# Optimization experiments

Measured on AMD Instinct MI355X. Metric: run time of the kernel, lower is better.

## Reference

```python
import math
import jax, jax.numpy as jnp
import numpy as np

N_NODES = 50000
N_EDGES = 600000
D = 128          # in_dim == out_dim
T = 4            # num_types
R = 4            # num_relations
H = 8            # n_heads
DK = D // H
MAX_LEN = 240    # RelTemporalEncoding max_len
EPS = 1e-5


def _sinusoid_table(n_hid, max_len):
    pos = jnp.arange(max_len, dtype=jnp.float32)[:, None]
    div = jnp.exp(jnp.arange(0, n_hid, 2, dtype=jnp.float32) * (-math.log(10000.0) / n_hid))
    s = jnp.sin(pos * div) / math.sqrt(n_hid)
    c = jnp.cos(pos * div) / math.sqrt(n_hid)
    emb = jnp.zeros((max_len, n_hid), dtype=jnp.float32)
    emb = emb.at[:, 0::2].set(s).at[:, 1::2].set(c)
    return emb


def setup_inputs() -> dict:
    key = jax.random.key(0)
    ks = jax.random.split(key, 24)
    f32 = jnp.float32
    inp = {
        'node_inp': jax.random.normal(ks[0], (N_NODES, D), dtype=f32),
        'node_type': jax.random.randint(ks[1], (N_NODES,), 0, T),
        'edge_index': jax.random.randint(ks[2], (2, N_EDGES), 0, N_NODES),
        'edge_type': jax.random.randint(ks[3], (N_EDGES,), 0, R),
        'edge_time': jax.random.randint(ks[4], (N_EDGES,), 0, MAX_LEN),
        # per-type Linear weights stored as [T, in, out] (x @ W + b)
        'Wk': jax.random.normal(ks[5], (T, D, D), dtype=f32) * 0.05,
        'bk': jnp.zeros((T, D), dtype=f32),
        'Wq': jax.random.normal(ks[6], (T, D, D), dtype=f32) * 0.05,
        'bq': jnp.zeros((T, D), dtype=f32),
        'Wv': jax.random.normal(ks[7], (T, D, D), dtype=f32) * 0.05,
        'bv': jnp.zeros((T, D), dtype=f32),
        'Wa': jax.random.normal(ks[8], (T, D, D), dtype=f32) * 0.05,
        'ba': jnp.zeros((T, D), dtype=f32),
        'gamma': jnp.ones((T, D), dtype=f32),
        'beta': jnp.zeros((T, D), dtype=f32),
        'rel_pri': jnp.ones((R, H), dtype=f32),
        'rel_att': jax.random.normal(ks[9], (R, H, DK, DK), dtype=f32) * 0.1,
        'rel_msg': jax.random.normal(ks[10], (R, H, DK, DK), dtype=f32) * 0.1,
        'skip': jnp.ones((T,), dtype=f32),
        'rte_W': jax.random.normal(ks[11], (D, D), dtype=f32) * 0.05,
        'rte_b': jnp.zeros((D,), dtype=f32),
    }
    return inp


def _type_proj(x, W, b, types):
    # all-type projection [T, N, D] then gather per-node type (T is small)
    allp = jnp.einsum('ni,tio->tno', x, W) + b[:, None, :]
    return allp[types, jnp.arange(x.shape[0])]


def reference(node_inp, node_type, edge_index, edge_type, edge_time,
              Wk, bk, Wq, bq, Wv, bv, Wa, ba, gamma, beta,
              rel_pri, rel_att, rel_msg, skip, rte_W, rte_b):
    N = node_inp.shape[0]
    E = edge_index.shape[1]
    src, tgt = edge_index[0], edge_index[1]  # j (source) -> i (target)

    # --- RelTemporalEncoding: x + Linear(emb[t]); emb is a fixed sinusoid table
    rte_out = _sinusoid_table(D, MAX_LEN) @ rte_W + rte_b  # [240, D]

    # --- per-node type-specific K/Q/V (linearity: K_t(x + rte) = K_t(x) + rte @ Wk_t)
    k_node = _type_proj(node_inp, Wk, bk, node_type)  # [N, D]
    v_node = _type_proj(node_inp, Wv, bv, node_type)
    q_node = _type_proj(node_inp, Wq, bq, node_type)
    k_rte = jnp.einsum('mi,tio->tmo', rte_out, Wk)  # [T, 240, D] (no bias; already in k_node)
    v_rte = jnp.einsum('mi,tio->tmo', rte_out, Wv)

    stype = node_type[src]
    k_e = (k_node[src] + k_rte[stype, edge_time]).reshape(E, H, DK)
    v_e = (v_node[src] + v_rte[stype, edge_time]).reshape(E, H, DK)
    q_e = q_node[tgt].reshape(E, H, DK)

    # --- per-relation head-wise transforms (R is small, fixed loop)
    k2 = jnp.zeros_like(k_e)
    msg = jnp.zeros_like(v_e)
    for r in range(R):
        sel = (edge_type == r)[:, None, None]
        k2 = jnp.where(sel, jnp.einsum('ehk,hkd->ehd', k_e, rel_att[r]), k2)
        msg = jnp.where(sel, jnp.einsum('ehk,hkd->ehd', v_e, rel_msg[r]), msg)

    logits = (q_e * k2).sum(-1) * rel_pri[edge_type] / math.sqrt(DK)  # [E, H]

    # --- softmax over edges grouped by target node
    m = jax.ops.segment_max(logits, tgt, num_segments=N)
    ex = jnp.exp(logits - m[tgt])
    den = jax.ops.segment_sum(ex, tgt, num_segments=N)
    att = ex / den[tgt]  # [E, H]

    res = (msg * att[..., None]).reshape(E, D)
    aggr = jax.ops.segment_sum(res, tgt, num_segments=N)  # [N, D]

    # --- update: per-type FFN + gated skip + per-type LayerNorm
    a = jax.nn.gelu(aggr, approximate=False)
    trans = _type_proj(a, Wa, ba, node_type)  # dropout p used in eval mode -> identity
    alpha = jax.nn.sigmoid(skip)[node_type][:, None]
    h = trans * alpha + node_inp * (1.0 - alpha)
    mu = h.mean(-1, keepdims=True)
    var = ((h - mu) ** 2).mean(-1, keepdims=True)
    out = (h - mu) / jnp.sqrt(var + EPS) * gamma[node_type] + beta[node_type]
    return out
```

## Files before the change

kernel.cpp:

```cpp
#include <hip/hip_runtime.h>
#include <hip/hip_fp16.h>
#include <math.h>

#define NH 8
#define NT 4
#define NR 4
#define MAXLEN 240

typedef __attribute__((ext_vector_type(8))) short bf16x8;
typedef __attribute__((ext_vector_type(4))) float f32x4;
typedef __attribute__((ext_vector_type(2))) float f32x2;

#if defined(__has_builtin)
#if __has_builtin(__builtin_amdgcn_cvt_pk_f32_fp8) && __has_builtin(__builtin_amdgcn_cvt_pk_fp8_f32)
#define HAS_HW_FP8 1
#endif
#endif

__device__ __forceinline__ unsigned short f2bf(float x) {
    unsigned u = __float_as_uint(x);
    u += 0x7fffu + ((u >> 16) & 1u);
    return (unsigned short)(u >> 16);
}
__device__ __forceinline__ float bflo(unsigned u) { return __uint_as_float(u << 16); }
__device__ __forceinline__ float bfhi(unsigned u) { return __uint_as_float(u & 0xffff0000u); }
__device__ __forceinline__ unsigned pack2(float a, float b) {
    return (unsigned)f2bf(a) | ((unsigned)f2bf(b) << 16);
}

__device__ __forceinline__ void fp8x4_dec(unsigned w, float* f) {
#ifdef HAS_HW_FP8
    f32x2 lo = __builtin_amdgcn_cvt_pk_f32_fp8(w, false);
    f32x2 hi = __builtin_amdgcn_cvt_pk_f32_fp8(w, true);
    f[0] = lo[0]; f[1] = lo[1]; f[2] = hi[0]; f[3] = hi[1];
#else
    unsigned ev = w & 0x00ff00ffu;
    unsigned od = (w >> 8) & 0x00ff00ffu;
    unsigned he = (((ev << 8) & 0x80008000u) | ((ev << 7) & 0x3f803f80u)) + 0x04000400u;
    unsigned ho = (((od << 8) & 0x80008000u) | ((od << 7) & 0x3f803f80u)) + 0x04000400u;
    __half2 h2e = *reinterpret_cast<__half2*>(&he);
    __half2 h2o = *reinterpret_cast<__half2*>(&ho);
    float2 fe = __half22float2(h2e);
    float2 fo = __half22float2(h2o);
    f[0] = fe.x; f[1] = fo.x; f[2] = fe.y; f[3] = fo.y;
#endif
}
__device__ __forceinline__ unsigned fp8x2_enc(float a, float b) {
#ifdef HAS_HW_FP8
    return (unsigned)__builtin_amdgcn_cvt_pk_fp8_f32(a, b, 0, false) & 0xffffu;
#else
    auto enc1 = [](float x) -> unsigned {
        float cl = fminf(fmaxf(x, -448.f), 448.f);
        __half h = __float2half(cl * 0.00390625f);
        unsigned short hr = *reinterpret_cast<unsigned short*>(&h);
        unsigned short rnd = (unsigned short)((hr & 0x7fff) + 0x3f + ((hr >> 7) & 1));
        return (unsigned)(((rnd >> 7) & 0x7f) | ((hr >> 8) & 0x80));
    };
    return enc1(a) | (enc1(b) << 8);
#endif
}

__global__ void zero_kernel(int* deg, int* cursor, int* dcnt, int* dcur, int N) {
    int i = blockIdx.x * blockDim.x + threadIdx.x;
    int stride = gridDim.x * blockDim.x;
    if (i < 256) { dcnt[i] = 0; dcur[i] = 0; }
    for (int j = i; j < N; j += stride) { deg[j] = 0; cursor[j] = 0; }
}

__global__ void deg_kernel(const int* __restrict__ ei, int* __restrict__ deg, int E) {
    int i = blockIdx.x * blockDim.x + threadIdx.x;
    int stride = gridDim.x * blockDim.x;
    for (int e = i; e < E; e += stride) atomicAdd(&deg[ei[E + e]], 1);
}

__global__ __launch_bounds__(256) void histA(const int* __restrict__ ntype,
                                             const int* __restrict__ deg,
                                             int* __restrict__ dcnt, int N) {
    __shared__ int h[256];
    int tid = threadIdx.x;
    h[tid] = 0;
    __syncthreads();
    int i = blockIdx.x * 256 + tid;
    if (i < N) atomicAdd(&h[ntype[i] * 64 + 63 - min(deg[i], 63)], 1);
    __syncthreads();
    if (h[tid]) atomicAdd(&dcnt[tid], h[tid]);
}

__global__ __launch_bounds__(256) void histB(const int* __restrict__ dcnt,
                                             int* __restrict__ dbase) {
    __shared__ int tmp[256];
    int v = dcnt[threadIdx.x];
    tmp[threadIdx.x] = v;
    __syncthreads();
    #pragma unroll
    for (int off = 1; off < 256; off <<= 1) {
        int t = threadIdx.x >= off ? tmp[threadIdx.x - off] : 0;
        __syncthreads();
        tmp[threadIdx.x] += t;
        __syncthreads();
    }
    dbase[threadIdx.x] = tmp[threadIdx.x] - v;
}

__global__ __launch_bounds__(256) void histC(const int* __restrict__ ntype,
                                             const int* __restrict__ deg,
                                             const int* __restrict__ dbase, int* __restrict__ dcur,
                                             int* __restrict__ nlist, int* __restrict__ spos,
                                             int* __restrict__ stype_s, int* __restrict__ deg_s,
                                             int N) {
    __shared__ int h[256];
    __shared__ int bb[256];
    __shared__ int cur[256];
    int tid = threadIdx.x;
    h[tid] = 0; cur[tid] = 0;
    __syncthreads();
    int i = blockIdx.x * 256 + tid;
    int b = -1, t = 0, dg = 0;
    if (i < N) {
        t = ntype[i]; dg = deg[i];
        b = t * 64 + 63 - min(dg, 63);
        atomicAdd(&h[b], 1);
    }
    __syncthreads();
    if (h[tid]) bb[tid] = atomicAdd(&dcur[tid], h[tid]);
    __syncthreads();
    if (i < N) {
        int r = atomicAdd(&cur[b], 1);
        int p = dbase[b] + bb[b] + r;
        nlist[p] = i;
        spos[i] = p;
        stype_s[p] = t;
        deg_s[p] = dg;
    }
}

__global__ __launch_bounds__(256) void scanA(const int* __restrict__ deg, int* __restrict__ excl,
                                             int* __restrict__ bsum, int N) {
    __shared__ int tmp[256];
    int i = blockIdx.x * 256 + threadIdx.x;
    int v = i < N ? deg[i] : 0;
    tmp[threadIdx.x] = v;
    __syncthreads();
    #pragma unroll
    for (int off = 1; off < 256; off <<= 1) {
        int t = threadIdx.x >= off ? tmp[threadIdx.x - off] : 0;
        __syncthreads();
        tmp[threadIdx.x] += t;
        __syncthreads();
    }
    if (i < N) excl[i] = tmp[threadIdx.x] - v;
    if (threadIdx.x == 255) bsum[blockIdx.x] = tmp[255];
}

__global__ __launch_bounds__(256) void scanB(int* __restrict__ bsum, int nb) {
    __shared__ int tmp[256];
    int v = threadIdx.x < nb ? bsum[threadIdx.x] : 0;
    tmp[threadIdx.x] = v;
    __syncthreads();
    #pragma unroll
    for (int off = 1; off < 256; off <<= 1) {
        int t = threadIdx.x >= off ? tmp[threadIdx.x - off] : 0;
        __syncthreads();
        tmp[threadIdx.x] += t;
        __syncthreads();
    }
    if (threadIdx.x < nb) bsum[threadIdx.x] = tmp[threadIdx.x] - v;
}

__global__ void scanC(const int* __restrict__ excl, const int* __restrict__ bsum,
                      int* __restrict__ row_start, int N) {
    int i = blockIdx.x * blockDim.x + threadIdx.x;
    if (i < N) row_start[i] = excl[i] + bsum[i >> 8];
}

__global__ void scatter_kernel(const int* __restrict__ ei, const int* __restrict__ etype,
                               const int* __restrict__ etime, const int* __restrict__ spos,
                               const int* __restrict__ dbase,
                               const int* __restrict__ row_start, int* __restrict__ cursor,
                               unsigned* __restrict__ ebuf, int E) {
    int tb1 = dbase[64], tb2 = dbase[128], tb3 = dbase[192];
    int i = blockIdx.x * blockDim.x + threadIdx.x;
    int stride = gridDim.x * blockDim.x;
    for (int e = i; e < E; e += stride) {
        int sps = spos[ei[e]];
        int spt = spos[ei[E + e]];
        int st = (sps >= tb1) + (sps >= tb2) + (sps >= tb3);
        int pos = atomicAdd(&cursor[spt], 1);
        ebuf[row_start[spt] + pos] =
            (unsigned)sps | ((unsigned)etype[e] << 17) | ((unsigned)etime[e] << 19) | ((unsigned)st << 27);
    }
}

__global__ __launch_bounds__(128) void rte_tables(
    const float* __restrict__ rte_W, const float* __restrict__ rte_b,
    const float* __restrict__ Wk, const float* __restrict__ Wv,
    const float* __restrict__ rel_msg,
    unsigned char* __restrict__ rtec8) {
    int m = blockIdx.x, t = blockIdx.y, d = threadIdx.x;
    __shared__ float emb[128];
    __shared__ float sr[128];
    __shared__ float vr[128];
    int j2 = d & ~1;
    float div = expf((float)j2 * (-9.210340371976184f / 128.f));
    float ang = (float)m * div;
    emb[d] = ((d & 1) ? cosf(ang) : sinf(ang)) * 0.08838834764831845f;
    __syncthreads();
    float ro = rte_b[d];
    #pragma unroll 8
    for (int i = 0; i < 128; ++i) ro += emb[i] * rte_W[i * 128 + d];
    sr[d] = ro;
    __syncthreads();
    float ak = 0.f, av = 0.f;
    for (int i = 0; i < 128; ++i) {
        float rv = sr[i];
        ak += rv * Wk[(t * 128 + i) * 128 + d];
        av += rv * Wv[(t * 128 + i) * 128 + d];
    }
    unsigned char kb = (unsigned char)(fp8x2_enc(fminf(fmaxf(ak, -440.f), 440.f), 0.f) & 0xff);
    int koff = (d >> 3) * 16 + 8 + (d & 7);
    #pragma unroll
    for (int r = 0; r < NR; ++r)
        rtec8[(size_t)((t * 4 + r) * MAXLEN + m) * 256 + koff] = kb;
    vr[d] = av;
    __syncthreads();
    int h = d >> 4, dd = d & 15;
    int voff = (d >> 3) * 16 + (d & 7);
    for (int r = 0; r < NR; ++r) {
        float acc = 0.f;
        #pragma unroll
        for (int k = 0; k < 16; ++k)
            acc += vr[h * 16 + k] * rel_msg[((r * NH + h) * 16 + k) * 16 + dd];
        unsigned char vb = (unsigned char)(fp8x2_enc(fminf(fmaxf(acc, -440.f), 440.f), 0.f) & 0xff);
        rtec8[(size_t)((t * 4 + r) * MAXLEN + m) * 256 + voff] = vb;
    }
}

__global__ __launch_bounds__(256) void pack_w9(
    const float* __restrict__ Wk, const float* __restrict__ Wq,
    const float* __restrict__ Wv, const float* __restrict__ Wa,
    const float* __restrict__ bk, const float* __restrict__ bq,
    const float* __restrict__ bv, const float* __restrict__ ba,
    const float* __restrict__ rel_att, const float* __restrict__ rel_msg,
    const float* __restrict__ rel_pri,
    short* __restrict__ PW2, float* __restrict__ PB) {
    if (blockIdx.x >= 320) {
        int bidx = (blockIdx.x - 320) * 256 + threadIdx.x;
        int col = bidx & 127, t = (bidx >> 7) & 3, set = bidx >> 9;
        int h = col >> 4, kk = col & 15;
        float val;
        if (set == 0) val = bk[t * 128 + col];
        else if (set == 9) val = ba[t * 128 + col];
        else if (set <= 4) {
            int r = set - 1;
            float pri = rel_pri[r * NH + h] * 0.25f;
            float acc = 0.f;
            #pragma unroll
            for (int dp = 0; dp < 16; ++dp)
                acc += bq[t * 128 + h * 16 + dp] * rel_att[((r * NH + h) * 16 + kk) * 16 + dp];
            val = acc * pri;
        } else {
            int r = set - 5;
            float acc = 0.f;
            #pragma unroll
            for (int kp = 0; kp < 16; ++kp)
                acc += bv[t * 128 + h * 16 + kp] * rel_msg[((r * NH + h) * 16 + kp) * 16 + kk];
            val = acc;
        }
        PB[bidx] = val;
        return;
    }
    int idx = blockIdx.x * 256 + threadIdx.x;
    int lane = idx & 63;
    int ks = (idx >> 6) & 3;
    int ctg = (idx >> 8) & 7;
    int t = (idx >> 11) & 3;
    int set = idx >> 13;
    int col = ctg * 16 + (lane & 15);
    int k0 = ks * 32 + (lane >> 4) * 8;
    int h = col >> 4, kk = col & 15;
    unsigned short o[8];
    if (set == 0 || set == 9) {
        const float* W = (set == 0 ? Wk : Wa) + t * 16384;
        #pragma unroll
        for (int j = 0; j < 8; ++j) o[j] = f2bf(W[(k0 + j) * 128 + col]);
    } else if (set <= 4) {
        int r = set - 1;
        float pri = rel_pri[r * NH + h] * 0.25f;
        float Ar[16];
        #pragma unroll
        for (int dp = 0; dp < 16; ++dp)
            Ar[dp] = rel_att[((r * NH + h) * 16 + kk) * 16 + dp] * pri;
        #pragma unroll
        for (int j = 0; j < 8; ++j) {
            const float* wr = Wq + (size_t)(t * 128 + k0 + j) * 128 + h * 16;
            float acc = 0.f;
            #pragma unroll
            for (int dp = 0; dp < 16; ++dp) acc += wr[dp] * Ar[dp];
            o[j] = f2bf(acc);
        }
    } else {
        int r = set - 5;
        float Mc[16];
        #pragma unroll
        for (int kp = 0; kp < 16; ++kp)
            Mc[kp] = rel_msg[((r * NH + h) * 16 + kp) * 16 + kk];
        #pragma unroll
        for (int j = 0; j < 8; ++j) {
            const float* wr = Wv + (size_t)(t * 128 + k0 + j) * 128 + h * 16;
            float acc = 0.f;
            #pragma unroll
            for (int kp = 0; kp < 16; ++kp) acc += wr[kp] * Mc[kp];
            o[j] = f2bf(acc);
        }
    }
    uint4 pk;
    pk.x = (unsigned)o[0] | ((unsigned)o[1] << 16);
    pk.y = (unsigned)o[2] | ((unsigned)o[3] << 16);
    pk.z = (unsigned)o[4] | ((unsigned)o[5] << 16);
    pk.w = (unsigned)o[6] | ((unsigned)o[7] << 16);
    *reinterpret_cast<uint4*>(PW2 + (size_t)idx * 8) = pk;
}

#define S8 144
#define S16 136
#define KST 144

__global__ __launch_bounds__(256, 4) void kqv2(
    const float* __restrict__ x, const int* __restrict__ nlist_,
    const int* __restrict__ stype_s, const short* __restrict__ PW2,
    const float* __restrict__ PB,
    unsigned char* __restrict__ knvm8, unsigned short* __restrict__ qa_s, int N) {
    __shared__ short af_l[2][4][64][8];
    __shared__ unsigned char ob8[32 * 272];
    __shared__ unsigned char kn_keep[32 * KST];
    __shared__ int st_l[32];
    unsigned short* ob16 = reinterpret_cast<unsigned short*>(ob8);
    const int tid = threadIdx.x;
    const int sp0 = blockIdx.x * 32;
    if (tid < 32) {
        int sp = sp0 + tid;
        st_l[tid] = stype_s[sp < N ? sp : N - 1];
    }
    {
        int i = tid >> 3;
        int d0 = (tid & 7) * 16;
        int sp = sp0 + i;
        int nid = nlist_[sp < N ? sp : N - 1];
        const float* xr = x + (size_t)nid * 128 + d0;
        float4 f0 = *reinterpret_cast<const float4*>(xr);
        float4 f1 = *reinterpret_cast<const float4*>(xr + 4);
        float4 f2 = *reinterpret_cast<const float4*>(xr + 8);
        float4 f3 = *reinterpret_cast<const float4*>(xr + 12);
        int m = i >> 4, rr = i & 15;
        int ks = d0 >> 5;
        int sub = (d0 >> 3) & 3;
        uint4 p0, p1;
        p0.x = pack2(f0.x, f0.y); p0.y = pack2(f0.z, f0.w);
        p0.z = pack2(f1.x, f1.y); p0.w = pack2(f1.z, f1.w);
        p1.x = pack2(f2.x, f2.y); p1.y = pack2(f2.z, f2.w);
        p1.z = pack2(f3.x, f3.y); p1.w = pack2(f3.z, f3.w);
        *reinterpret_cast<uint4*>(&af_l[m][ks][sub * 16 + rr][0]) = p0;
        *reinterpret_cast<uint4*>(&af_l[m][ks][(sub + 1) * 16 + rr][0]) = p1;
    }
    __syncthreads();

    const int lane = tid & 63, w = tid >> 6;
    const int col_l = lane & 15, rowg = lane >> 4;
    const int t0 = st_l[0], t1 = st_l[31];

    bf16x8 afr[2][4];
    #pragma unroll
    for (int m = 0; m < 2; ++m)
        #pragma unroll
        for (int ks = 0; ks < 4; ++ks)
            afr[m][ks] = *reinterpret_cast<const bf16x8*>(&af_l[m][ks][lane][0]);

    for (int set = 0; set < 9; ++set) {
        bool isf8 = (set == 0 || set >= 5);
        for (int t = t0; t <= t1; ++t) {
            #pragma unroll
            for (int c = 0; c < 2; ++c) {
                int ctg = w + c * 4;
                bf16x8 pf[4];
                #pragma unroll
                for (int ks = 0; ks < 4; ++ks)
                    pf[ks] = *reinterpret_cast<const bf16x8*>(
                        PW2 + ((size_t)((((set * 4 + t) * 8 + ctg) * 4 + ks) * 64 + lane)) * 8);
                float bval = PB[(set * 4 + t) * 128 + ctg * 16 + col_l];
                #pragma unroll
                for (int m = 0; m < 2; ++m) {
                    f32x4 acc = {0.f, 0.f, 0.f, 0.f};
                    #pragma unroll
                    for (int ks = 0; ks < 4; ++ks)
                        acc = __builtin_amdgcn_mfma_f32_16x16x32_bf16(afr[m][ks], pf[ks], acc, 0, 0, 0);
                    if (isf8) {
                        float c0 = fminf(fmaxf(acc[0] + bval, -440.f), 440.f);
                        float c1 = fminf(fmaxf(acc[1] + bval, -440.f), 440.f);
                        float c2 = fminf(fmaxf(acc[2] + bval, -440.f), 440.f);
                        float c3 = fminf(fmaxf(acc[3] + bval, -440.f), 440.f);
                        unsigned pA = fp8x2_enc(c0, c1);
                        unsigned pB = fp8x2_enc(c2, c3);
                        unsigned char by[4];
                        by[0] = (unsigned char)(pA & 0xff);
                        by[1] = (unsigned char)((pA >> 8) & 0xff);
                        by[2] = (unsigned char)(pB & 0xff);
                        by[3] = (unsigned char)((pB >> 8) & 0xff);
                        #pragma unroll
                        for (int j = 0; j < 4; ++j) {
                            int i = m * 16 + rowg * 4 + j;
                            if (st_l[i] == t)
                                ob8[i * S8 + ctg * 16 + col_l] = by[j];
                        }
                    } else {
                        #pragma unroll
                        for (int j = 0; j < 4; ++j) {
                            int i = m * 16 + rowg * 4 + j;
                            if (st_l[i] == t)
                                ob16[i * S16 + ctg * 16 + col_l] = f2bf(acc[j] + bval);
                        }
                    }
                }
            }
        }
        __syncthreads();
        if (set == 0) {
            int i = tid >> 3, seg = tid & 7;
            *reinterpret_cast<uint4*>(&kn_keep[i * KST + seg * 16]) =
                *reinterpret_cast<const uint4*>(&ob8[i * S8 + seg * 16]);
        } else if (set >= 5) {
            int i = tid >> 3, seg = tid & 7;
            int sp = sp0 + i;
            if (sp < N) {
                int r = set - 5;
                unsigned char* dst = knvm8 + (size_t)(sp * 4 + r) * 256;
                #pragma unroll
                for (int cc = 0; cc < 2; ++cc) {
                    int c = seg * 2 + cc;
                    uint2 vmc = *reinterpret_cast<const uint2*>(&ob8[i * S8 + c * 8]);
                    uint2 knc = *reinterpret_cast<const uint2*>(&kn_keep[i * KST + c * 8]);
                    uint4 outv;
                    outv.x = vmc.x; outv.y = vmc.y; outv.z = knc.x; outv.w = knc.y;
                    *reinterpret_cast<uint4*>(dst + c * 16) = outv;
                }
            }
        } else {
            int i = tid >> 3, d0 = (tid & 7) * 16;
            int sp = sp0 + i;
            if (sp < N) {
                unsigned short* dst = qa_s + ((size_t)sp * 4 + (set - 1)) * 128;
                const unsigned short* src = ob16 + i * S16 + d0;
                *reinterpret_cast<uint4*>(dst + d0) = *reinterpret_cast<const uint4*>(src);
                *reinterpret_cast<uint4*>(dst + d0 + 8) = *reinterpret_cast<const uint4*>(src + 8);
            }
        }
        __syncthreads();
    }
}

__global__ __launch_bounds__(256) void fused_edge_attn(
    const unsigned* __restrict__ ebuf, const int* __restrict__ row_start,
    const int* __restrict__ deg_s,
    const unsigned char* __restrict__ knvm8, const unsigned char* __restrict__ rtec8,
    const unsigned short* __restrict__ qa_s,
    unsigned short* __restrict__ aggr_bf, int N) {
    int sp = blockIdx.x * 16 + (threadIdx.x >> 4);
    int l16 = threadIdx.x & 15;
    if (sp >= N) return;
    uint4 q[4];
    #pragma unroll
    for (int r = 0; r < 4; ++r)
        q[r] = *reinterpret_cast<const uint4*>(qa_s + ((size_t)sp * 4 + r) * 128 + l16 * 8);
    int start = row_start[sp], cnt = deg_s[sp];
    float den = 0.f;
    float acc[8] = {0.f, 0.f, 0.f, 0.f, 0.f, 0.f, 0.f, 0.f};
    int i = 0;
    for (; i + 2 <= cnt; i += 2) {
        unsigned e0 = ebuf[start + i];
        unsigned e1 = ebuf[start + i + 1];
        int sps0 = e0 & 0x1ffff, r0 = (e0 >> 17) & 3, tm0 = (e0 >> 19) & 255, st0 = (e0 >> 27) & 3;
        int sps1 = e1 & 0x1ffff, r1 = (e1 >> 17) & 3, tm1 = (e1 >> 19) & 255, st1 = (e1 >> 27) & 3;
        uint4 g10 = *reinterpret_cast<const uint4*>(knvm8 + (size_t)(sps0 * 4 + r0) * 256 + l16 * 16);
        uint4 g20 = *reinterpret_cast<const uint4*>(rtec8 + (size_t)((st0 * 4 + r0) * MAXLEN + tm0) * 256 + l16 * 16);
        uint4 g11 = *reinterpret_cast<const uint4*>(knvm8 + (size_t)(sps1 * 4 + r1) * 256 + l16 * 16);
        uint4 g21 = *reinterpret_cast<const uint4*>(rtec8 + (size_t)((st1 * 4 + r1) * MAXLEN + tm1) * 256 + l16 * 16);
        float mf0[8], kf0[8], mr0[8], kr0[8];
        float mf1[8], kf1[8], mr1[8], kr1[8];
        fp8x4_dec(g10.x, mf0); fp8x4_dec(g10.y, mf0 + 4);
        fp8x4_dec(g10.z, kf0); fp8x4_dec(g10.w, kf0 + 4);
        fp8x4_dec(g20.x, mr0); fp8x4_dec(g20.y, mr0 + 4);
        fp8x4_dec(g20.z, kr0); fp8x4_dec(g20.w, kr0 + 4);
        fp8x4_dec(g11.x, mf1); fp8x4_dec(g11.y, mf1 + 4);
        fp8x4_dec(g11.z, kf1); fp8x4_dec(g11.w, kf1 + 4);
        fp8x4_dec(g21.x, mr1); fp8x4_dec(g21.y, mr1 + 4);
        fp8x4_dec(g21.z, kr1); fp8x4_dec(g21.w, kr1 + 4);
        uint4 q0 = q[r0], q1 = q[r1];
        float p0 = (kf0[0] + kr0[0]) * bflo(q0.x) + (kf0[1] + kr0[1]) * bfhi(q0.x)
                 + (kf0[2] + kr0[2]) * bflo(q0.y) + (kf0[3] + kr0[3]) * bfhi(q0.y)
                 + (kf0[4] + kr0[4]) * bflo(q0.z) + (kf0[5] + kr0[5]) * bfhi(q0.z)
                 + (kf0[6] + kr0[6]) * bflo(q0.w) + (kf0[7] + kr0[7]) * bfhi(q0.w);
        float p1 = (kf1[0] + kr1[0]) * bflo(q1.x) + (kf1[1] + kr1[1]) * bfhi(q1.x)
                 + (kf1[2] + kr1[2]) * bflo(q1.y) + (kf1[3] + kr1[3]) * bfhi(q1.y)
                 + (kf1[4] + kr1[4]) * bflo(q1.z) + (kf1[5] + kr1[5]) * bfhi(q1.z)
                 + (kf1[6] + kr1[6]) * bflo(q1.w) + (kf1[7] + kr1[7]) * bfhi(q1.w);
        p0 += __shfl_xor(p0, 1);
        p1 += __shfl_xor(p1, 1);
        float w0 = __expf(p0), w1 = __expf(p1);
        den += w0 + w1;
        #pragma unroll
        for (int j = 0; j < 8; ++j)
            acc[j] += w0 * (mf0[j] + mr0[j]) + w1 * (mf1[j] + mr1[j]);
    }
    if (i < cnt) {
        unsigned e0 = ebuf[start + i];
        int sps0 = e0 & 0x1ffff, r0 = (e0 >> 17) & 3, tm0 = (e0 >> 19) & 255, st0 = (e0 >> 27) & 3;
        uint4 g10 = *reinterpret_cast<const uint4*>(knvm8 + (size_t)(sps0 * 4 + r0) * 256 + l16 * 16);
        uint4 g20 = *reinterpret_cast<const uint4*>(rtec8 + (size_t)((st0 * 4 + r0) * MAXLEN + tm0) * 256 + l16 * 16);
        float mf0[8], kf0[8], mr0[8], kr0[8];
        fp8x4_dec(g10.x, mf0); fp8x4_dec(g10.y, mf0 + 4);
        fp8x4_dec(g10.z, kf0); fp8x4_dec(g10.w, kf0 + 4);
        fp8x4_dec(g20.x, mr0); fp8x4_dec(g20.y, mr0 + 4);
        fp8x4_dec(g20.z, kr0); fp8x4_dec(g20.w, kr0 + 4);
        uint4 q0 = q[r0];
        float p0 = (kf0[0] + kr0[0]) * bflo(q0.x) + (kf0[1] + kr0[1]) * bfhi(q0.x)
                 + (kf0[2] + kr0[2]) * bflo(q0.y) + (kf0[3] + kr0[3]) * bfhi(q0.y)
                 + (kf0[4] + kr0[4]) * bflo(q0.z) + (kf0[5] + kr0[5]) * bfhi(q0.z)
                 + (kf0[6] + kr0[6]) * bflo(q0.w) + (kf0[7] + kr0[7]) * bfhi(q0.w);
        p0 += __shfl_xor(p0, 1);
        float w0 = __expf(p0);
        den += w0;
        #pragma unroll
        for (int j = 0; j < 8; ++j)
            acc[j] += w0 * (mf0[j] + mr0[j]);
    }
    float inv = den > 0.f ? 1.f / den : 0.f;
    uint4 o;
    o.x = pack2(acc[0] * inv, acc[1] * inv);
    o.y = pack2(acc[2] * inv, acc[3] * inv);
    o.z = pack2(acc[4] * inv, acc[5] * inv);
    o.w = pack2(acc[6] * inv, acc[7] * inv);
    *reinterpret_cast<uint4*>(aggr_bf + (size_t)sp * 128 + l16 * 8) = o;
}

__global__ __launch_bounds__(256, 4) void update_sorted(
    const float* __restrict__ x, const int* __restrict__ nlist_,
    const int* __restrict__ stype_s, const short* __restrict__ PW2,
    const float* __restrict__ PB, const float* __restrict__ gamma,
    const float* __restrict__ beta, const float* __restrict__ skip,
    const unsigned short* __restrict__ aggr_bf, float* __restrict__ out, int N) {
    __shared__ short af_l[2][4][64][8];
    __shared__ float hs[32][128];
    __shared__ int st_l[32];
    __shared__ int nid_l[32];
    const int tid = threadIdx.x;
    const int sp0 = blockIdx.x * 32;
    if (tid < 32) {
        int sp = sp0 + tid;
        int spc = sp < N ? sp : N - 1;
        st_l[tid] = stype_s[spc];
        nid_l[tid] = nlist_[spc];
    }
    {
        int i = tid >> 3;
        int d0 = (tid & 7) * 16;
        int spc = sp0 + i < N ? sp0 + i : N - 1;
        const unsigned short* ar = aggr_bf + (size_t)spc * 128 + d0;
        uint4 v0 = *reinterpret_cast<const uint4*>(ar);
        uint4 v1 = *reinterpret_cast<const uint4*>(ar + 8);
        unsigned vv[8] = {v0.x, v0.y, v0.z, v0.w, v1.x, v1.y, v1.z, v1.w};
        float g[16];
        #pragma unroll
        for (int c = 0; c < 8; ++c) {
            float a0 = bflo(vv[c]), a1 = bfhi(vv[c]);
            g[c * 2 + 0] = 0.5f * a0 * (1.f + erff(a0 * 0.7071067811865476f));
            g[c * 2 + 1] = 0.5f * a1 * (1.f + erff(a1 * 0.7071067811865476f));
        }
        int m = i >> 4, rr = i & 15;
        int ks = d0 >> 5;
        int sub = (d0 >> 3) & 3;
        uint4 p0, p1;
        p0.x = pack2(g[0], g[1]);  p0.y = pack2(g[2], g[3]);
        p0.z = pack2(g[4], g[5]);  p0.w = pack2(g[6], g[7]);
        p1.x = pack2(g[8], g[9]);  p1.y = pack2(g[10], g[11]);
        p1.z = pack2(g[12], g[13]); p1.w = pack2(g[14], g[15]);
        *reinterpret_cast<uint4*>(&af_l[m][ks][sub * 16 + rr][0]) = p0;
        *reinterpret_cast<uint4*>(&af_l[m][ks][(sub + 1) * 16 + rr][0]) = p1;
    }
    __syncthreads();

    const int lane = tid & 63, w = tid >> 6;
    const int col_l = lane & 15, rowg = lane >> 4;
    const int t0 = st_l[0], t1 = st_l[31];

    bf16x8 afr[2][4];
    #pragma unroll
    for (int m = 0; m < 2; ++m)
        #pragma unroll
        for (int ks = 0; ks < 4; ++ks)
            afr[m][ks] = *reinterpret_cast<const bf16x8*>(&af_l[m][ks][lane][0]);

    for (int t = t0; t <= t1; ++t) {
        #pragma unroll
        for (int c = 0; c < 2; ++c) {
            int ctg = w + c * 4;
            bf16x8 pf[4];
            #pragma unroll
            for (int ks = 0; ks < 4; ++ks)
                pf[ks] = *reinterpret_cast<const bf16x8*>(
                    PW2 + ((size_t)((((9 * 4 + t) * 8 + ctg) * 4 + ks) * 64 + lane)) * 8);
            float bval = PB[(9 * 4 + t) * 128 + ctg * 16 + col_l];
            #pragma unroll
            for (int m = 0; m < 2; ++m) {
                f32x4 acc = {0.f, 0.f, 0.f, 0.f};
                #pragma unroll
                for (int ks = 0; ks < 4; ++ks)
                    acc = __builtin_amdgcn_mfma_f32_16x16x32_bf16(afr[m][ks], pf[ks], acc, 0, 0, 0);
                #pragma unroll
                for (int j = 0; j < 4; ++j) {
                    int i = m * 16 + rowg * 4 + j;
                    if (st_l[i] == t)
                        hs[i][ctg * 16 + col_l] = acc[j] + bval;
                }
            }
        }
    }
    __syncthreads();

    {
        int i = tid >> 3;
        int d0 = (tid & 7) * 16;
        int sp = sp0 + i;
        int nid = nid_l[i];
        int t = st_l[i];
        float alpha = 1.f / (1.f + expf(-skip[t]));
        const float* xr = x + (size_t)nid * 128 + d0;
        float hv[16];
        float s1 = 0.f, s2 = 0.f;
        #pragma unroll
        for (int c = 0; c < 4; ++c) {
            float4 xf = *reinterpret_cast<const float4*>(xr + c * 4);
            float4 tf;
            tf.x = hs[i][d0 + c * 4 + 0]; tf.y = hs[i][d0 + c * 4 + 1];
            tf.z = hs[i][d0 + c * 4 + 2]; tf.w = hs[i][d0 + c * 4 + 3];
            hv[c * 4 + 0] = tf.x * alpha + xf.x * (1.f - alpha);
            hv[c * 4 + 1] = tf.y * alpha + xf.y * (1.f - alpha);
            hv[c * 4 + 2] = tf.z * alpha + xf.z * (1.f - alpha);
            hv[c * 4 + 3] = tf.w * alpha + xf.w * (1.f - alpha);
            #pragma unroll
            for (int j = 0; j < 4; ++j) { s1 += hv[c * 4 + j]; s2 += hv[c * 4 + j] * hv[c * 4 + j]; }
        }
        #pragma unroll
        for (int off = 1; off < 8; off <<= 1) {
            s1 += __shfl_xor(s1, off);
            s2 += __shfl_xor(s2, off);
        }
        float mu = s1 * (1.f / 128.f);
        float var = s2 * (1.f / 128.f) - mu * mu;
        float inv = 1.f / sqrtf(var + 1e-5f);
        if (sp < N) {
            float* orow = out + (size_t)nid * 128 + d0;
            const float* gr = gamma + t * 128 + d0;
            const float* br = beta + t * 128 + d0;
            #pragma unroll
            for (int c = 0; c < 4; ++c) {
                float4 gf = *reinterpret_cast<const float4*>(gr + c * 4);
                float4 bf = *reinterpret_cast<const float4*>(br + c * 4);
                float4 of;
                of.x = (hv[c * 4 + 0] - mu) * inv * gf.x + bf.x;
                of.y = (hv[c * 4 + 1] - mu) * inv * gf.y + bf.y;
                of.z = (hv[c * 4 + 2] - mu) * inv * gf.z + bf.z;
                of.w = (hv[c * 4 + 3] - mu) * inv * gf.w + bf.w;
                *reinterpret_cast<float4*>(orow + c * 4) = of;
            }
        }
    }
}

extern "C" void kernel_launch(void* const* d_in, const int* in_sizes, int n_in,
                              void* d_out, int out_size, void* d_ws, size_t ws_size,
                              hipStream_t stream) {
    const float* node_inp = (const float*)d_in[0];
    const int*   node_type = (const int*)d_in[1];
    const int*   edge_index = (const int*)d_in[2];
    const int*   edge_type = (const int*)d_in[3];
    const int*   edge_time = (const int*)d_in[4];
    const float* Wk = (const float*)d_in[5];
    const float* bk = (const float*)d_in[6];
    const float* Wq = (const float*)d_in[7];
    const float* bq = (const float*)d_in[8];
    const float* Wv = (const float*)d_in[9];
    const float* bv = (const float*)d_in[10];
    const float* Wa = (const float*)d_in[11];
    const float* ba = (const float*)d_in[12];
    const float* gamma = (const float*)d_in[13];
    const float* beta = (const float*)d_in[14];
    const float* rel_pri = (const float*)d_in[15];
    const float* rel_att = (const float*)d_in[16];
    const float* rel_msg = (const float*)d_in[17];
    const float* skip = (const float*)d_in[18];
    const float* rte_W = (const float*)d_in[19];
    const float* rte_b = (const float*)d_in[20];

    int N = in_sizes[0] / 128;
    int E = in_sizes[3];

    char* base = (char*)d_ws;
    unsigned char* knvm8 = (unsigned char*)base;      base += (size_t)N * 4 * 256;
    unsigned short* qa_s = (unsigned short*)base;     base += (size_t)N * 4 * 128 * 2;
    unsigned short* aggr_bf = (unsigned short*)base;  base += (size_t)N * 128 * 2;
    unsigned char* rtec8 = (unsigned char*)base;      base += (size_t)NT * NR * MAXLEN * 256;
    short* PW2 = (short*)base;                base += (size_t)10 * NT * 128 * 128 * 2;
    float* PB = (float*)base;                 base += (size_t)10 * NT * 128 * 4;
    int* deg = (int*)base;                    base += (size_t)N * 4;
    int* deg_s = (int*)base;                  base += (size_t)N * 4;
    int* cursor = (int*)base;                 base += (size_t)N * 4;
    int* excl = (int*)base;                   base += (size_t)N * 4;
    int* row_start = (int*)base;              base += (size_t)N * 4;
    int* nlist = (int*)base;                  base += (size_t)N * 4;
    int* spos = (int*)base;                   base += (size_t)N * 4;
    int* stype_s = (int*)base;                base += (size_t)N * 4;
    int* bsum = (int*)base;                   base += 256 * 4;
    int* dcnt = (int*)base;                   base += 256 * 4;
    int* dcur = (int*)base;                   base += 256 * 4;
    int* dbase = (int*)base;                  base += 256 * 4;
    base = (char*)(((size_t)base + 15) & ~(size_t)15);
    unsigned* ebuf = (unsigned*)base;         base += (size_t)E * 4;

    int nb = (N + 255) / 256;
    int ng = (N + 255) / 256;

    zero_kernel<<<256, 256, 0, stream>>>(deg, cursor, dcnt, dcur, N);
    deg_kernel<<<1024, 256, 0, stream>>>(edge_index, deg, E);
    histA<<<ng, 256, 0, stream>>>(node_type, deg, dcnt, N);
    histB<<<1, 256, 0, stream>>>(dcnt, dbase);
    histC<<<ng, 256, 0, stream>>>(node_type, deg, dbase, dcur, nlist, spos, stype_s, deg_s, N);
    scanA<<<nb, 256, 0, stream>>>(deg_s, excl, bsum, N);
    scanB<<<1, 256, 0, stream>>>(bsum, nb);
    scanC<<<nb, 256, 0, stream>>>(excl, bsum, row_start, N);
    scatter_kernel<<<1024, 256, 0, stream>>>(edge_index, edge_type, edge_time, spos, dbase,
                                             row_start, cursor, ebuf, E);
    dim3 gt(MAXLEN, NT);
    rte_tables<<<gt, 128, 0, stream>>>(rte_W, rte_b, Wk, Wv, rel_msg, rtec8);
    pack_w9<<<340, 256, 0, stream>>>(Wk, Wq, Wv, Wa, bk, bq, bv, ba,
                                     rel_att, rel_msg, rel_pri, PW2, PB);
    kqv2<<<(N + 31) / 32, 256, 0, stream>>>(node_inp, nlist, stype_s, PW2, PB,
                                            knvm8, qa_s, N);
    fused_edge_attn<<<(N + 15) / 16, 256, 0, stream>>>(ebuf, row_start, deg_s,
                                                       knvm8, rtec8, qa_s, aggr_bf, N);
    update_sorted<<<(N + 31) / 32, 256, 0, stream>>>(node_inp, nlist, stype_s, PW2, PB,
                                                     gamma, beta, skip, aggr_bf, (float*)d_out, N);
}
```

Measured before the change: 238.7 us.

## Store per-relation query projections in fp8 and double-buffer the kqv2 staging tile

The four per-relation query projections are now written as fp8 instead of bf16, halving that intermediate buffer, and the edge kernel decodes them back to bf16 on load. The kqv2 staging buffer is double-buffered by set parity, which removes the second barrier per set iteration. This cuts global write and read traffic for the q tensor and some synchronisation, at the cost of reduced precision on the attention logits and extra decode work per node.

```diff
diff --git a/kernel.cpp b/kernel.cpp
--- a/kernel.cpp
+++ b/kernel.cpp
@@ -322,19 +322,17 @@
 }
 
 #define S8 144
-#define S16 136
 #define KST 144
 
 __global__ __launch_bounds__(256, 4) void kqv2(
     const float* __restrict__ x, const int* __restrict__ nlist_,
     const int* __restrict__ stype_s, const short* __restrict__ PW2,
     const float* __restrict__ PB,
-    unsigned char* __restrict__ knvm8, unsigned short* __restrict__ qa_s, int N) {
+    unsigned char* __restrict__ knvm8, unsigned char* __restrict__ qa8, int N) {
     __shared__ short af_l[2][4][64][8];
-    __shared__ unsigned char ob8[32 * 272];
+    __shared__ unsigned char obuf[2][32 * S8];
     __shared__ unsigned char kn_keep[32 * KST];
     __shared__ int st_l[32];
-    unsigned short* ob16 = reinterpret_cast<unsigned short*>(ob8);
     const int tid = threadIdx.x;
     const int sp0 = blockIdx.x * 32;
     if (tid < 32) {
@@ -375,8 +373,11 @@
         for (int ks = 0; ks < 4; ++ks)
             afr[m][ks] = *reinterpret_cast<const bf16x8*>(&af_l[m][ks][lane][0]);
 
+    const int wi = tid >> 3, wseg = tid & 7;
+    const int wsp = sp0 + wi;
+
     for (int set = 0; set < 9; ++set) {
-        bool isf8 = (set == 0 || set >= 5);
+        unsigned char* buf = &obuf[set & 1][0];
         for (int t = t0; t <= t1; ++t) {
             #pragma unroll
             for (int c = 0; c < 2; ++c) {
@@ -393,67 +394,51 @@
                     #pragma unroll
                     for (int ks = 0; ks < 4; ++ks)
                         acc = __builtin_amdgcn_mfma_f32_16x16x32_bf16(afr[m][ks], pf[ks], acc, 0, 0, 0);
-                    if (isf8) {
-                        float c0 = fminf(fmaxf(acc[0] + bval, -440.f), 440.f);
-                        float c1 = fminf(fmaxf(acc[1] + bval, -440.f), 440.f);
-                        float c2 = fminf(fmaxf(acc[2] + bval, -440.f), 440.f);
-                        float c3 = fminf(fmaxf(acc[3] + bval, -440.f), 440.f);
-                        unsigned pA = fp8x2_enc(c0, c1);
-                        unsigned pB = fp8x2_enc(c2, c3);
-                        unsigned char by[4];
-                        by[0] = (unsigned char)(pA & 0xff);
-                        by[1] = (unsigned char)((pA >> 8) & 0xff);
-                        by[2] = (unsigned char)(pB & 0xff);
-                        by[3] = (unsigned char)((pB >> 8) & 0xff);
-                        #pragma unroll
-                        for (int j = 0; j < 4; ++j) {
-                            int i = m * 16 + rowg * 4 + j;
-                            if (st_l[i] == t)
-                                ob8[i * S8 + ctg * 16 + col_l] = by[j];
-                        }
-                    } else {
-                        #pragma unroll
-                        for (int j = 0; j < 4; ++j) {
-                            int i = m * 16 + rowg * 4 + j;
-                            if (st_l[i] == t)
-                                ob16[i * S16 + ctg * 16 + col_l] = f2bf(acc[j] + bval);
-                        }
+                    float c0 = fminf(fmaxf(acc[0] + bval, -440.f), 440.f);
+                    float c1 = fminf(fmaxf(acc[1] + bval, -440.f), 440.f);
+                    float c2 = fminf(fmaxf(acc[2] + bval, -440.f), 440.f);
+                    float c3 = fminf(fmaxf(acc[3] + bval, -440.f), 440.f);
+                    unsigned pA = fp8x2_enc(c0, c1);
+                    unsigned pB = fp8x2_enc(c2, c3);
+                    unsigned char by[4];
+                    by[0] = (unsigned char)(pA & 0xff);
+                    by[1] = (unsigned char)((pA >> 8) & 0xff);
+                    by[2] = (unsigned char)(pB & 0xff);
+                    by[3] = (unsigned char)((pB >> 8) & 0xff);
+                    #pragma unroll
+                    for (int j = 0; j < 4; ++j) {
+                        int i = m * 16 + rowg * 4 + j;
+                        if (st_l[i] == t)
+                            buf[i * S8 + ctg * 16 + col_l] = by[j];
                     }
                 }
             }
         }
         __syncthreads();
         if (set == 0) {
-            int i = tid >> 3, seg = tid & 7;
-            *reinterpret_cast<uint4*>(&kn_keep[i * KST + seg * 16]) =
-                *reinterpret_cast<const uint4*>(&ob8[i * S8 + seg * 16]);
-        } else if (set >= 5) {
-            int i = tid >> 3, seg = tid & 7;
-            int sp = sp0 + i;
-            if (sp < N) {
+            *reinterpret_cast<uint4*>(&kn_keep[wi * KST + wseg * 16]) =
+                *reinterpret_cast<const uint4*>(&buf[wi * S8 + wseg * 16]);
+        } else if (set <= 4) {
+            if (wsp < N) {
+                int r = set - 1;
+                *reinterpret_cast<uint4*>(qa8 + (size_t)(wsp * 4 + r) * 128 + wseg * 16) =
+                    *reinterpret_cast<const uint4*>(&buf[wi * S8 + wseg * 16]);
+            }
+        } else {
+            if (wsp < N) {
                 int r = set - 5;
-                unsigned char* dst = knvm8 + (size_t)(sp * 4 + r) * 256;
+                unsigned char* dst = knvm8 + (size_t)(wsp * 4 + r) * 256;
                 #pragma unroll
                 for (int cc = 0; cc < 2; ++cc) {
-                    int c = seg * 2 + cc;
-                    uint2 vmc = *reinterpret_cast<const uint2*>(&ob8[i * S8 + c * 8]);
-                    uint2 knc = *reinterpret_cast<const uint2*>(&kn_keep[i * KST + c * 8]);
+                    int c = wseg * 2 + cc;
+                    uint2 vmc = *reinterpret_cast<const uint2*>(&buf[wi * S8 + c * 8]);
+                    uint2 knc = *reinterpret_cast<const uint2*>(&kn_keep[wi * KST + c * 8]);
                     uint4 outv;
                     outv.x = vmc.x; outv.y = vmc.y; outv.z = knc.x; outv.w = knc.y;
                     *reinterpret_cast<uint4*>(dst + c * 16) = outv;
                 }
             }
-        } else {
-            int i = tid >> 3, d0 = (tid & 7) * 16;
-            int sp = sp0 + i;
-            if (sp < N) {
-                unsigned short* dst = qa_s + ((size_t)sp * 4 + (set - 1)) * 128;
-                const unsigned short* src = ob16 + i * S16 + d0;
-                *reinterpret_cast<uint4*>(dst + d0) = *reinterpret_cast<const uint4*>(src);
-                *reinterpret_cast<uint4*>(dst + d0 + 8) = *reinterpret_cast<const uint4*>(src + 8);
-            }
-        }
-        __syncthreads();
+        }
     }
 }
 
@@ -461,15 +446,20 @@
     const unsigned* __restrict__ ebuf, const int* __restrict__ row_start,
     const int* __restrict__ deg_s,
     const unsigned char* __restrict__ knvm8, const unsigned char* __restrict__ rtec8,
-    const unsigned short* __restrict__ qa_s,
+    const unsigned char* __restrict__ qa8,
     unsigned short* __restrict__ aggr_bf, int N) {
     int sp = blockIdx.x * 16 + (threadIdx.x >> 4);
     int l16 = threadIdx.x & 15;
     if (sp >= N) return;
     uint4 q[4];
     #pragma unroll
-    for (int r = 0; r < 4; ++r)
-        q[r] = *reinterpret_cast<const uint4*>(qa_s + ((size_t)sp * 4 + r) * 128 + l16 * 8);
+    for (int r = 0; r < 4; ++r) {
+        uint2 qv = *reinterpret_cast<const uint2*>(qa8 + (size_t)(sp * 4 + r) * 128 + l16 * 8);
+        float f[8];
+        fp8x4_dec(qv.x, f); fp8x4_dec(qv.y, f + 4);
+        q[r].x = pack2(f[0], f[1]); q[r].y = pack2(f[2], f[3]);
+        q[r].z = pack2(f[4], f[5]); q[r].w = pack2(f[6], f[7]);
+    }
     int start = row_start[sp], cnt = deg_s[sp];
     float den = 0.f;
     float acc[8] = {0.f, 0.f, 0.f, 0.f, 0.f, 0.f, 0.f, 0.f};
@@ -705,7 +695,7 @@
 
     char* base = (char*)d_ws;
     unsigned char* knvm8 = (unsigned char*)base;      base += (size_t)N * 4 * 256;
-    unsigned short* qa_s = (unsigned short*)base;     base += (size_t)N * 4 * 128 * 2;
+    unsigned char* qa8 = (unsigned char*)base;        base += (size_t)N * 4 * 128;
     unsigned short* aggr_bf = (unsigned short*)base;  base += (size_t)N * 128 * 2;
     unsigned char* rtec8 = (unsigned char*)base;      base += (size_t)NT * NR * MAXLEN * 256;
     short* PW2 = (short*)base;                base += (size_t)10 * NT * 128 * 128 * 2;
@@ -743,9 +733,9 @@
     pack_w9<<<340, 256, 0, stream>>>(Wk, Wq, Wv, Wa, bk, bq, bv, ba,
                                      rel_att, rel_msg, rel_pri, PW2, PB);
     kqv2<<<(N + 31) / 32, 256, 0, stream>>>(node_inp, nlist, stype_s, PW2, PB,
-                                            knvm8, qa_s, N);
+                                            knvm8, qa8, N);
     fused_edge_attn<<<(N + 15) / 16, 256, 0, stream>>>(ebuf, row_start, deg_s,
-                                                       knvm8, rtec8, qa_s, aggr_bf, N);
+                                                       knvm8, rtec8, qa8, aggr_bf, N);
     update_sorted<<<(N + 31) / 32, 256, 0, stream>>>(node_inp, nlist, stype_s, PW2, PB,
                                                      gamma, beta, skip, aggr_bf, (float*)d_out, N);
 }
```

Result: faster. 217.1 us (-9.0%).
